# Optimization experiments

Measured on AMD Instinct MI355X. Metric: run time of the kernel, lower is better.

Reference implementation:

```python
import jax, jax.numpy as jnp
import numpy as np

N = 131072
K = 27
FIN = 3
FOUT = 32
EPS = 1e-5


def _bn(h, gamma, beta, mean, var):
    return (h - mean) * jax.lax.rsqrt(var + EPS) * gamma + beta


def setup_inputs() -> dict:
    key = jax.random.key(0)
    ks = jax.random.split(key, 8)
    return {
        "x_feats": jax.random.normal(ks[0], (N, FIN), jnp.float32),
        "z_feats": jax.random.normal(ks[1], (N, FIN), jnp.float32),
        "nbr_idx": jax.random.randint(ks[2], (N, K), 0, N, jnp.int32),
        "w1": jax.random.normal(ks[3], (K, FIN, FOUT), jnp.float32) * 0.2,
        "bn1_gamma": jnp.ones((FOUT,), jnp.float32),
        "bn1_beta": jnp.zeros((FOUT,), jnp.float32),
        "bn1_mean": jax.random.normal(ks[4], (FOUT,), jnp.float32) * 0.1,
        "bn1_var": jax.random.uniform(ks[5], (FOUT,), jnp.float32, 0.5, 1.5),
        "w2": jax.random.normal(ks[6], (K, FOUT, FOUT), jnp.float32) * 0.1,
        "mlp_w": jax.random.normal(ks[7], (FIN, FOUT), jnp.float32) * 0.3,
        "mlp_b": jnp.zeros((FOUT,), jnp.float32),
        "mlp_gamma": jnp.ones((FOUT,), jnp.float32),
        "mlp_beta": jnp.zeros((FOUT,), jnp.float32),
        "mlp_mean": jnp.zeros((FOUT,), jnp.float32),
        "mlp_var": jnp.ones((FOUT,), jnp.float32),
    }


def reference(x_feats, z_feats, nbr_idx, w1, bn1_gamma, bn1_beta, bn1_mean,
              bn1_var, w2, mlp_w, mlp_b, mlp_gamma, mlp_beta, mlp_mean,
              mlp_var):
    # --- voxel branch: sparse conv (gather-GEMM) -> BN -> SiLU -> sparse conv
    g1 = x_feats[nbr_idx]                       # [N, K, FIN] irregular gather
    h = jnp.einsum('nkf,kfo->no', g1, w1)       # [N, FOUT]
    h = jax.nn.silu(_bn(h, bn1_gamma, bn1_beta, bn1_mean, bn1_var))
    g2 = h[nbr_idx]                             # [N, K, FOUT] irregular gather
    x_out = jnp.einsum('nkf,kfo->no', g2, w2)   # [N, FOUT]

    # --- point branch: SharedMLP = Linear -> BN -> ReLU
    z = z_feats @ mlp_w + mlp_b
    z = jax.nn.relu(_bn(z, mlp_gamma, mlp_beta, mlp_mean, mlp_var))

    # --- mixed_mix: fuse voxel and point features additively
    fused = x_out + z
    return (fused, fused)
```

## Files before the change

### kernel.cpp

```cpp
#include <hip/hip_runtime.h>
#include <math.h>

#define NN 131072
#define KK 27
#define FIN 3
#define FOUT 32
#define EPS 1e-5f

typedef _Float16 f16;
typedef __attribute__((ext_vector_type(8))) _Float16 f16x8;
typedef __attribute__((ext_vector_type(16))) float f32x16;

__global__ __launch_bounds__(256) void pack_x_kernel(
    const float* __restrict__ x, float4* __restrict__ xp)
{
    const int n = blockIdx.x * 256 + threadIdx.x;
    if (n < NN)
        xp[n] = make_float4(x[n * 3], x[n * 3 + 1], x[n * 3 + 2], 0.f);
}

__global__ __launch_bounds__(256) void pack_w2_kernel(
    const float* __restrict__ w2, f16* __restrict__ w2p)
{
    const int t = blockIdx.x * 256 + threadIdx.x;
    if (t >= KK * 2 * 64 * 8) return;
    const int k    = t >> 10;
    const int rem  = t & 1023;
    const int half = rem >> 9;
    const int l    = (rem >> 3) & 63;
    const int j    = rem & 7;
    const int krow = half * 16 + ((l >> 5) << 3) + j;
    const int n    = l & 31;
    w2p[t] = (f16)w2[k * (FOUT * FOUT) + krow * FOUT + n];
}

__global__ __launch_bounds__(256) void conv1_kernel(
    const float4* __restrict__ xp,
    const int*   __restrict__ nbr_idx,
    const float* __restrict__ w1,
    const float* __restrict__ g1,  const float* __restrict__ b1,
    const float* __restrict__ m1,  const float* __restrict__ v1,
    f16* __restrict__ h_out)
{
    const int n = blockIdx.x * 256 + threadIdx.x;

    int idxs[KK];
    const int* nb = nbr_idx + (size_t)n * KK;
#pragma unroll
    for (int k = 0; k < KK; ++k) idxs[k] = nb[k];

    float acc[FOUT];
#pragma unroll
    for (int o = 0; o < FOUT; ++o) acc[o] = 0.f;

#pragma unroll
    for (int c = 0; c < 3; ++c) {
        float4 xs[9];
#pragma unroll
        for (int q = 0; q < 9; ++q)
            xs[q] = xp[idxs[c * 9 + q]];
#pragma unroll
        for (int q = 0; q < 9; ++q) {
            const float* w = w1 + (c * 9 + q) * (FIN * FOUT);
#pragma unroll
            for (int o = 0; o < FOUT; ++o) {
                float a = acc[o];
                a = fmaf(xs[q].x, w[o],            a);
                a = fmaf(xs[q].y, w[FOUT + o],     a);
                a = fmaf(xs[q].z, w[2 * FOUT + o], a);
                acc[o] = a;
            }
        }
    }

    f16* hr = h_out + (size_t)n * FOUT;
#pragma unroll
    for (int g = 0; g < 4; ++g) {
        f16x8 hv;
#pragma unroll
        for (int j = 0; j < 8; ++j) {
            const int o = g * 8 + j;
            const float sc = g1[o] * rsqrtf(v1[o] + EPS);
            float v = (acc[o] - m1[o]) * sc + b1[o];
            v = v / (1.f + __expf(-v));
            hv[j] = (f16)v;
        }
        *(f16x8*)(hr + g * 8) = hv;
    }
}

__global__ __launch_bounds__(256) void conv2_mfma_kernel(
    const f16*   __restrict__ h,
    const int*   __restrict__ nbr_idx,
    const f16*   __restrict__ w2p,
    const float* __restrict__ z_feats,
    const float* __restrict__ mlp_w,
    const float* __restrict__ mlp_b,
    const float* __restrict__ mg, const float* __restrict__ mbe,
    const float* __restrict__ mm, const float* __restrict__ mv,
    float* __restrict__ out)
{
    const int lane = threadIdx.x & 63;
    const int wave = threadIdx.x >> 6;
    const int base = (blockIdx.x * 4 + wave) * 32;
    const int row  = lane & 31;
    const int hi   = lane >> 5;

    int idxs[KK];
    const int* nb = nbr_idx + (size_t)(base + row) * KK;
#pragma unroll
    for (int k = 0; k < KK; ++k) idxs[k] = nb[k];

    f32x16 acc = {};

    const f16x8* bp = (const f16x8*)w2p;
#pragma unroll 3
    for (int k = 0; k < KK; ++k) {
        const f16* hr = h + (size_t)idxs[k] * FOUT + hi * 8;
        const f16x8 a1 = *(const f16x8*)hr;
        const f16x8 a2 = *(const f16x8*)(hr + 16);
        const f16x8 b1 = bp[k * 128 + lane];
        const f16x8 b2 = bp[k * 128 + 64 + lane];
        acc = __builtin_amdgcn_mfma_f32_32x32x16_f16(a1, b1, acc, 0, 0, 0);
        acc = __builtin_amdgcn_mfma_f32_32x32x16_f16(a2, b2, acc, 0, 0, 0);
    }

    const int n0 = lane & 31;
    const float wc0 = mlp_w[n0];
    const float wc1 = mlp_w[FOUT + n0];
    const float wc2 = mlp_w[2 * FOUT + n0];
    const float sc  = mg[n0] * rsqrtf(mv[n0] + EPS);
    const float bi  = mlp_b[n0];
    const float mmv = mm[n0];
    const float mbv = mbe[n0];

#pragma unroll
    for (int r = 0; r < 16; ++r) {
        const int m    = (r & 3) + ((r >> 2) << 3) + (hi << 2);
        const int node = base + m;
        const float* zr = z_feats + (size_t)node * FIN;
        float z = bi;
        z = fmaf(zr[0], wc0, z);
        z = fmaf(zr[1], wc1, z);
        z = fmaf(zr[2], wc2, z);
        z = (z - mmv) * sc + mbv;
        z = fmaxf(z, 0.f);
        const float v = acc[r] + z;
        out[(size_t)node * FOUT + n0] = v;
        out[(size_t)NN * FOUT + (size_t)node * FOUT + n0] = v;
    }
}

extern "C" void kernel_launch(void* const* d_in, const int* in_sizes, int n_in,
                              void* d_out, int out_size, void* d_ws, size_t ws_size,
                              hipStream_t stream) {
    const float* x_feats = (const float*)d_in[0];
    const float* z_feats = (const float*)d_in[1];
    const int*   nbr_idx = (const int*)d_in[2];
    const float* w1      = (const float*)d_in[3];
    const float* bn1_g   = (const float*)d_in[4];
    const float* bn1_b   = (const float*)d_in[5];
    const float* bn1_m   = (const float*)d_in[6];
    const float* bn1_v   = (const float*)d_in[7];
    const float* w2      = (const float*)d_in[8];
    const float* mlp_w   = (const float*)d_in[9];
    const float* mlp_b   = (const float*)d_in[10];
    const float* mlp_g   = (const float*)d_in[11];
    const float* mlp_be  = (const float*)d_in[12];
    const float* mlp_m   = (const float*)d_in[13];
    const float* mlp_v   = (const float*)d_in[14];

    f16*    h   = (f16*)d_ws;
    f16*    w2p = (f16*)((char*)d_ws + (size_t)8 * 1024 * 1024);
    float4* xp  = (float4*)((char*)d_ws + (size_t)9 * 1024 * 1024);
    float*  out = (float*)d_out;

    pack_x_kernel<<<NN / 256, 256, 0, stream>>>(x_feats, xp);
    pack_w2_kernel<<<(KK * 1024 + 255) / 256, 256, 0, stream>>>(w2, w2p);
    conv1_kernel<<<NN / 256, 256, 0, stream>>>(xp, nbr_idx, w1,
                                               bn1_g, bn1_b, bn1_m, bn1_v, h);
    conv2_mfma_kernel<<<NN / 128, 256, 0, stream>>>(h, nbr_idx, w2p, z_feats,
                                                    mlp_w, mlp_b, mlp_g, mlp_be,
                                                    mlp_m, mlp_v, out);
}
```

Before: 169.1 us.

## Restructure conv1 to cooperatively gather neighbors into LDS and split outputs across waves

conv1 now processes 64 nodes per block. All 256 threads cooperatively load the neighbor indices with coalesced reads and gather the packed x features into shared memory. Each of the 4 waves then computes 8 of the 32 output channels for the 64 nodes, which cuts per-thread registers and raises parallelism. The cost is LDS usage (about 27 KB per block), a barrier, and LDS reads with stride 27 float4 that may cause bank conflicts.

Result: slower. 172.6 us (+2.1%).

```diff
diff --git a/kernel.cpp b/kernel.cpp
--- a/kernel.cpp
+++ b/kernel.cpp
@@ -42,51 +42,62 @@
     const float* __restrict__ m1,  const float* __restrict__ v1,
     f16* __restrict__ h_out)
 {
-    const int n = blockIdx.x * 256 + threadIdx.x;
+    __shared__ float4 xs[64 * KK];
 
-    int idxs[KK];
-    const int* nb = nbr_idx + (size_t)n * KK;
+    const int tid  = threadIdx.x;
+    const int nb0  = blockIdx.x * 64;
+
+    const int* nb = nbr_idx + (size_t)nb0 * KK;
+    {
+        int   idxv[7];
+        float4 xv[7];
 #pragma unroll
-    for (int k = 0; k < KK; ++k) idxs[k] = nb[k];
+        for (int t = 0; t < 7; ++t) {
+            const int i = t * 256 + tid;
+            idxv[t] = (i < 64 * KK) ? nb[i] : 0;
+        }
+#pragma unroll
+        for (int t = 0; t < 7; ++t)
+            xv[t] = xp[idxv[t]];
+#pragma unroll
+        for (int t = 0; t < 7; ++t) {
+            const int i = t * 256 + tid;
+            if (i < 64 * KK) xs[i] = xv[t];
+        }
+    }
+    __syncthreads();
 
-    float acc[FOUT];
+    const int l  = tid & 63;
+    const int ob = __builtin_amdgcn_readfirstlane((tid >> 6) * 8);
+
+    float acc[8];
 #pragma unroll
-    for (int o = 0; o < FOUT; ++o) acc[o] = 0.f;
+    for (int o = 0; o < 8; ++o) acc[o] = 0.f;
 
+#pragma unroll 9
+    for (int k = 0; k < KK; ++k) {
+        const float4 xv = xs[l * KK + k];
+        const float* w = w1 + k * (FIN * FOUT) + ob;
 #pragma unroll
-    for (int c = 0; c < 3; ++c) {
-        float4 xs[9];
-#pragma unroll
-        for (int q = 0; q < 9; ++q)
-            xs[q] = xp[idxs[c * 9 + q]];
-#pragma unroll
-        for (int q = 0; q < 9; ++q) {
-            const float* w = w1 + (c * 9 + q) * (FIN * FOUT);
-#pragma unroll
-            for (int o = 0; o < FOUT; ++o) {
-                float a = acc[o];
-                a = fmaf(xs[q].x, w[o],            a);
-                a = fmaf(xs[q].y, w[FOUT + o],     a);
-                a = fmaf(xs[q].z, w[2 * FOUT + o], a);
-                acc[o] = a;
-            }
+        for (int o = 0; o < 8; ++o) {
+            float a = acc[o];
+            a = fmaf(xv.x, w[o],            a);
+            a = fmaf(xv.y, w[FOUT + o],     a);
+            a = fmaf(xv.z, w[2 * FOUT + o], a);
+            acc[o] = a;
         }
     }
 
-    f16* hr = h_out + (size_t)n * FOUT;
+    f16x8 hv;
 #pragma unroll
-    for (int g = 0; g < 4; ++g) {
-        f16x8 hv;
-#pragma unroll
-        for (int j = 0; j < 8; ++j) {
-            const int o = g * 8 + j;
-            const float sc = g1[o] * rsqrtf(v1[o] + EPS);
-            float v = (acc[o] - m1[o]) * sc + b1[o];
-            v = v / (1.f + __expf(-v));
-            hv[j] = (f16)v;
-        }
-        *(f16x8*)(hr + g * 8) = hv;
+    for (int j = 0; j < 8; ++j) {
+        const int o = ob + j;
+        const float sc = g1[o] * rsqrtf(v1[o] + EPS);
+        float v = (acc[j] - m1[o]) * sc + b1[o];
+        v = v / (1.f + __expf(-v));
+        hv[j] = (f16)v;
     }
+    *(f16x8*)(h_out + (size_t)(nb0 + l) * FOUT + ob) = hv;
 }
 
 __global__ __launch_bounds__(256) void conv2_mfma_kernel(
@@ -177,8 +188,8 @@
 
     pack_x_kernel<<<NN / 256, 256, 0, stream>>>(x_feats, xp);
     pack_w2_kernel<<<(KK * 1024 + 255) / 256, 256, 0, stream>>>(w2, w2p);
-    conv1_kernel<<<NN / 256, 256, 0, stream>>>(xp, nbr_idx, w1,
-                                               bn1_g, bn1_b, bn1_m, bn1_v, h);
+    conv1_kernel<<<NN / 64, 256, 0, stream>>>(xp, nbr_idx, w1,
+                                              bn1_g, bn1_b, bn1_m, bn1_v, h);
     conv2_mfma_kernel<<<NN / 128, 256, 0, stream>>>(h, nbr_idx, w2p, z_feats,
                                                     mlp_w, mlp_b, mlp_g, mlp_be,
                                                     mlp_m, mlp_v, out);
```
